# Kernel optimization log

Measured on AMD Instinct MI355X. Metric: run time of the kernel, lower is better.

## Reference

```python
import jax, jax.numpy as jnp
import numpy as np
from functools import partial

N_NODES = 100000
N_REL = 3
N_EDGES = 200000
IN_F = 128
HID_F = 128
OUT_F = 128
N_QUERY = 4096


def _graph_conv(x, es, ed, W, b, n_nodes):
    """DGL GraphConv with norm='both': D_dst^{-1/2} A D_src^{-1/2} X W + b.
    es/ed: [E] int edge endpoints, x: [N, d_in], W: [d_in, d_out], b: [d_out]."""
    ones = jnp.ones(es.shape[0], dtype=x.dtype)
    out_deg = jnp.clip(jax.ops.segment_sum(ones, es, num_segments=n_nodes), 1.0)
    in_deg = jnp.clip(jax.ops.segment_sum(ones, ed, num_segments=n_nodes), 1.0)
    # transform first (dense GEMM), then gather -> scatter-add over dst
    y = (x * jax.lax.rsqrt(out_deg)[:, None]) @ W          # [N, d_out]
    msg = y[es]                                            # [E, d_out] gather
    agg = jax.ops.segment_sum(msg, ed, num_segments=n_nodes)  # [N, d_out]
    return agg * jax.lax.rsqrt(in_deg)[:, None] + b


def _hetero_layer(x, e_src, e_dst, W, b, n_nodes):
    # HeteroGraphConv(aggregate='sum'): sum per-relation GraphConv outputs.
    out = _graph_conv(x, e_src[0], e_dst[0], W[0], b[0], n_nodes)
    for r in range(1, e_src.shape[0]):
        out = out + _graph_conv(x, e_src[r], e_dst[r], W[r], b[r], n_nodes)
    return out


def setup_inputs() -> dict:
    key = jax.random.key(0)
    ks = jax.random.split(key, 9)
    s = 1.0 / np.sqrt(IN_F)
    return {
        "emb": jax.random.normal(ks[0], (N_NODES, IN_F), jnp.float32),
        "W1": jax.random.normal(ks[1], (N_REL, IN_F, HID_F), jnp.float32) * s,
        "b1": jnp.zeros((N_REL, HID_F), jnp.float32),
        "W2": jax.random.normal(ks[2], (N_REL, HID_F, OUT_F), jnp.float32) * s,
        "b2": jnp.zeros((N_REL, OUT_F), jnp.float32),
        "e_src": jax.random.randint(ks[3], (N_REL, N_EDGES), 0, N_NODES, jnp.int32),
        "e_dst": jax.random.randint(ks[4], (N_REL, N_EDGES), 0, N_NODES, jnp.int32),
        "src": jax.random.randint(ks[5], (N_QUERY,), 0, N_NODES, jnp.int32),
        "dst": jax.random.randint(ks[6], (N_QUERY,), 0, N_NODES, jnp.int32),
    }


def reference(emb, W1, b1, W2, b2, e_src, e_dst, src, dst):
    n = emb.shape[0]
    h = jnp.tanh(_hetero_layer(emb, e_src, e_dst, W1, b1, n))
    h = jnp.tanh(_hetero_layer(h, e_src, e_dst, W2, b2, n))
    return (h[src], h[dst])
```

## Files before the change

### kernel.cpp

```cpp
#include <hip/hip_runtime.h>
#include <stdint.h>

#define NN 100000
#define NREL 3
#define NE 200000
#define F 128
#define NQ 4096

#define NBUCK (NREL * NN)
#define NCB ((NBUCK + 255) / 256)
#define CH_BLOCKS 512
#define CH_CHUNK ((NREL * NE + CH_BLOCKS - 1) / CH_BLOCKS)

#define WCVT_N (2 * NREL * F * F)
#define A1 (WCVT_N + 256)
#define A2 (A1 + NN * F / 8)
#define A3 (A2 + 2 * NQ)
#define A4 (A3 + NN)
#define A5 (A4 + NN)
#define PREP_N (A5 + 1)
#define PREP_BLKS ((PREP_N + 255) / 256)

typedef float fx4 __attribute__((ext_vector_type(4)));
typedef unsigned short u16x8 __attribute__((ext_vector_type(8)));
typedef __bf16 bf16x8 __attribute__((ext_vector_type(8)));

__device__ __forceinline__ unsigned short f2bf(float f) {
  uint32_t u = __builtin_bit_cast(uint32_t, f);
  uint32_t r = u + 0x7FFFu + ((u >> 16) & 1u);
  return (unsigned short)(r >> 16);
}
__device__ __forceinline__ float bf2f(unsigned short u) {
  return __builtin_bit_cast(float, (uint32_t)u << 16);
}
__device__ __forceinline__ int rel_of(int i) {
  return (i >= 2 * NE) ? 2 : (i >= NE ? 1 : 0);
}

__global__ __launch_bounds__(256) void prepch_kernel(
    const float* __restrict__ W1, const float* __restrict__ W2,
    const float* __restrict__ b1, const float* __restrict__ b2,
    const float* __restrict__ emb,
    const int* __restrict__ qsrc, const int* __restrict__ qdst,
    const int* __restrict__ es, const int* __restrict__ ed,
    unsigned short* __restrict__ Wtb, float* __restrict__ bsum,
    unsigned short* __restrict__ xb,
    int* __restrict__ qnode, int* __restrict__ mark, int* __restrict__ qflag,
    int* __restrict__ cursor,
    int* __restrict__ Hd, int* __restrict__ Hs) {
  __shared__ int hd[NCB], hs[NCB];
  int t = threadIdx.x;
  if (blockIdx.x >= PREP_BLKS) {
    int blk = blockIdx.x - PREP_BLKS;
    for (int j = t; j < NCB; j += 256) { hd[j] = 0; hs[j] = 0; }
    __syncthreads();
    int lo = blk * CH_CHUNK;
    int hi = min(lo + CH_CHUNK, NREL * NE);
    for (int i = lo + t; i < hi; i += 256) {
      int r = rel_of(i);
      atomicAdd(&hd[(r * NN + ed[i]) >> 8], 1);
      atomicAdd(&hs[(r * NN + es[i]) >> 8], 1);
    }
    __syncthreads();
    for (int j = t; j < NCB; j += 256) {
      Hd[blk * NCB + j] = hd[j];
      Hs[blk * NCB + j] = hs[j];
    }
    return;
  }
  int i = blockIdx.x * blockDim.x + t;
  if (i < WCVT_N) {
    int l = i / (NREL * F * F);
    int rem = i % (NREL * F * F);
    int r = rem / (F * F);
    int nk = rem % (F * F);
    int n = nk >> 7, k = nk & 127;
    const float* W = l ? W2 : W1;
    Wtb[i] = f2bf(W[r * F * F + k * F + n]);
  } else if (i < A1) {
    int tt = i - WCVT_N;
    int l = tt >> 7, f = tt & 127;
    const float* b = l ? b2 : b1;
    bsum[l * F + f] = b[f] + b[F + f] + b[2 * F + f];
  } else if (i < A2) {
    int j = i - A1;
    const float* p = emb + (size_t)j * 8;
    unsigned short tmp[8];
#pragma unroll
    for (int e = 0; e < 8; ++e) tmp[e] = f2bf(p[e]);
    *reinterpret_cast<u16x8*>(xb + (size_t)j * 8) = *reinterpret_cast<u16x8*>(tmp);
  } else if (i < A3) {
    int m = i - A2;
    qnode[m] = (m < NQ) ? qsrc[m] : qdst[m - NQ];
  } else if (i < A4) {
    mark[i - A3] = 0;
  } else if (i < A5) {
    qflag[i - A4] = 0;
  } else if (i < PREP_N) {
    *cursor = 0;
  }
}

__global__ __launch_bounds__(256) void hsum_kernel(const int* __restrict__ Hd,
                                                   const int* __restrict__ Hs,
                                                   const int* __restrict__ qnode,
                                                   int* __restrict__ chist_d,
                                                   int* __restrict__ chist_s,
                                                   int* __restrict__ qflag) {
  int t = threadIdx.x, lane = t & 63;
  int q = blockIdx.x * 256 + t;
  if (q < 2 * NQ) qflag[qnode[q]] = 1;
  int ws = blockIdx.x * 4 + (t >> 6);
  if (ws >= 2 * NCB) return;
  const int* H = (ws < NCB) ? Hd : Hs;
  int bin = (ws < NCB) ? ws : ws - NCB;
  int s = 0;
#pragma unroll
  for (int k = 0; k < 8; ++k) s += H[(size_t)(lane * 8 + k) * NCB + bin];
#pragma unroll
  for (int d = 1; d < 64; d <<= 1) s += __shfl_xor(s, d);
  if (lane == 0) {
    if (ws < NCB) chist_d[bin] = s; else chist_s[bin] = s;
  }
}

__global__ __launch_bounds__(256) void cscan_kernel(const int* __restrict__ chist_d,
                                                    const int* __restrict__ chist_s,
                                                    int* __restrict__ cstart_d,
                                                    int* __restrict__ cstart_s) {
  const int* chist = blockIdx.x ? chist_s : chist_d;
  int* cstart = blockIdx.x ? cstart_s : cstart_d;
  int t = threadIdx.x, lane = t & 63, w = t >> 6;
  int v[5];
  int s = 0;
#pragma unroll
  for (int k = 0; k < 5; ++k) {
    int i = t * 5 + k;
    v[k] = (i < NCB) ? chist[i] : 0;
    s += v[k];
  }
  int sc = s;
#pragma unroll
  for (int d = 1; d < 64; d <<= 1) {
    int o = __shfl_up(sc, d);
    if (lane >= d) sc += o;
  }
  __shared__ int wt[4];
  if (lane == 63) wt[w] = sc;
  __syncthreads();
  int woff = 0;
#pragma unroll
  for (int ww = 0; ww < 3; ++ww) woff += (ww < w) ? wt[ww] : 0;
  int excl = woff + sc - s;
#pragma unroll
  for (int k = 0; k < 5; ++k) {
    int i = t * 5 + k;
    if (i < NCB) { cstart[i] = excl; excl += v[k]; }
  }
}

__global__ __launch_bounds__(256) void hbase_kernel(const int* __restrict__ Hd,
                                                    const int* __restrict__ Hs,
                                                    const int* __restrict__ cstart_d,
                                                    const int* __restrict__ cstart_s,
                                                    int* __restrict__ Hbase_d,
                                                    int* __restrict__ Hbase_s) {
  const int* H = blockIdx.y ? Hs : Hd;
  const int* cstart = blockIdx.y ? cstart_s : cstart_d;
  int* Hbase = blockIdx.y ? Hbase_s : Hbase_d;
  int t = threadIdx.x, lane = t & 63;
  int bin = blockIdx.x * 4 + (t >> 6);
  int v[8];
  int s = 0;
#pragma unroll
  for (int k = 0; k < 8; ++k) {
    v[k] = H[(size_t)(lane * 8 + k) * NCB + bin];
    s += v[k];
  }
  int sc = s;
#pragma unroll
  for (int d = 1; d < 64; d <<= 1) {
    int o = __shfl_up(sc, d);
    if (lane >= d) sc += o;
  }
  int run = cstart[bin] + sc - s;
#pragma unroll
  for (int k = 0; k < 8; ++k) {
    Hbase[bin * CH_BLOCKS + lane * 8 + k] = run;
    run += v[k];
  }
}

__global__ __launch_bounds__(256) void cscatter_kernel(const int* __restrict__ es,
                                                       const int* __restrict__ ed,
                                                       const int* __restrict__ Hbase_d,
                                                       const int* __restrict__ Hbase_s,
                                                       int* __restrict__ etmp_d,
                                                       int* __restrict__ etmp_s) {
  __shared__ int cur_d[NCB], cur_s[NCB];
  int t = threadIdx.x, blk = blockIdx.x;
  for (int j = t; j < NCB; j += 256) {
    cur_d[j] = Hbase_d[j * CH_BLOCKS + blk];
    cur_s[j] = Hbase_s[j * CH_BLOCKS + blk];
  }
  __syncthreads();
  int lo = blk * CH_CHUNK;
  int hi = min(lo + CH_CHUNK, NREL * NE);
  for (int i = lo + t; i < hi; i += 256) {
    int r = rel_of(i);
    int s = es[i], d = ed[i];
    int bd = r * NN + d;
    int pos = atomicAdd(&cur_d[bd >> 8], 1);
    etmp_d[pos] = (s << 8) | (bd & 255);
    int bs = r * NN + s;
    int pos_s = atomicAdd(&cur_s[bs >> 8], 1);
    etmp_s[pos_s] = bs & 255;
  }
}

__global__ __launch_bounds__(256) void srccount_kernel(const int* __restrict__ etmp_s,
                                                       const int* __restrict__ cstart_s,
                                                       const int* __restrict__ chist_s,
                                                       int* __restrict__ cnt_src) {
  const int cb = blockIdx.x;
  const int t = threadIdx.x;
  const int cs = cstart_s[cb], cc = chist_s[cb];
  __shared__ int fcnt[256];
  fcnt[t] = 0;
  __syncthreads();
  for (int i = t; i < cc; i += 256) atomicAdd(&fcnt[etmp_s[cs + i]], 1);
  __syncthreads();
  int b = cb * 256 + t;
  if (b < NBUCK) cnt_src[b] = fcnt[t];
}

__global__ __launch_bounds__(256) void fine_kernel(const int* __restrict__ etmp,
                                                   const int* __restrict__ cstart,
                                                   const int* __restrict__ chist,
                                                   const int* __restrict__ cnt_src,
                                                   const int* __restrict__ qflag,
                                                   int2* __restrict__ scb,
                                                   int2* __restrict__ epay,
                                                   int* __restrict__ mark) {
  const int cb = blockIdx.x;
  const int t = threadIdx.x, lane = t & 63, w = t >> 6;
  const int cs = cstart[cb], cc = chist[cb];
  __shared__ int fcnt[256], fexcl[256], fcur[256];
  fcnt[t] = 0;
  fcur[t] = 0;
  __syncthreads();
  for (int i = t; i < cc; i += 256) atomicAdd(&fcnt[etmp[cs + i] & 255], 1);
  __syncthreads();
  int val = fcnt[t];
  int sc = val;
#pragma unroll
  for (int d = 1; d < 64; d <<= 1) {
    int o = __shfl_up(sc, d);
    if (lane >= d) sc += o;
  }
  __shared__ int wt[4];
  if (lane == 63) wt[w] = sc;
  __syncthreads();
  int woff = 0;
#pragma unroll
  for (int ww = 0; ww < 3; ++ww) woff += (ww < w) ? wt[ww] : 0;
  fexcl[t] = woff + sc - val;
  int b = cb * 256 + t;
  if (b < NBUCK) scb[b] = make_int2(cs + fexcl[t], val);
  __syncthreads();
  for (int i = t; i < cc; i += 256) {
    int e = etmp[cs + i];
    int f = e & 255;
    int src = ((unsigned)e) >> 8;
    int fine = cb * 256 + f;
    int r = fine / NN;
    int dst = fine - r * NN;
    float wgt = rsqrtf((float)cnt_src[r * NN + src]) * rsqrtf((float)fcnt[f]);
    int pos = cs + fexcl[f] + atomicAdd(&fcur[f], 1);
    epay[pos] = make_int2(src, __builtin_bit_cast(int, wgt));
    if (qflag[dst]) mark[src] = 1;
  }
}

__global__ __launch_bounds__(256) void compact_kernel(const int* __restrict__ mark,
                                                      int* __restrict__ list,
                                                      int* __restrict__ cursor) {
  int t = threadIdx.x, lane = t & 63, w = t >> 6;
  int base = blockIdx.x * 1024 + t * 4;
  int loc[4];
  int cnt = 0;
#pragma unroll
  for (int k = 0; k < 4; ++k) {
    int i = base + k;
    if (i < NN && mark[i]) { loc[cnt] = i; ++cnt; }
  }
  int sc = cnt;
#pragma unroll
  for (int d = 1; d < 64; d <<= 1) {
    int o = __shfl_up(sc, d);
    if (lane >= d) sc += o;
  }
  int texcl = sc - cnt;
  __shared__ int wt[4];
  __shared__ int bb;
  if (lane == 63) wt[w] = sc;
  __syncthreads();
  if (t == 0) {
    int tot = wt[0] + wt[1] + wt[2] + wt[3];
    bb = atomicAdd(cursor, tot);
    int a = 0;
#pragma unroll
    for (int ww = 0; ww < 4; ++ww) { int c = wt[ww]; wt[ww] = a; a += c; }
  }
  __syncthreads();
  int p = bb + wt[w] + texcl;
  for (int k = 0; k < cnt; ++k) list[p + k] = loc[k];
}

__global__ __launch_bounds__(256) void aggz_kernel(const unsigned short* __restrict__ X,
                                                   const int2* __restrict__ scb,
                                                   const int2* __restrict__ epay,
                                                   const int* __restrict__ nmap,
                                                   const int* __restrict__ cntp,
                                                   unsigned short* __restrict__ Z,
                                                   int Mcap, int Ms) {
  const int count = cntp ? *cntp : Mcap;
  const int r = blockIdx.y;
  const int t = threadIdx.x;
  const int lane = t & 63;
  const int m = blockIdx.x * 16 + (t >> 6) * 4 + (lane >> 4);
  const int j = lane & 15;
  if (m >= count) return;
  int n = nmap ? nmap[m] : m;
  int2 meta = scb[r * NN + n];
  const int2* ep = epay + meta.x;
  const int c = meta.y;

  float ps[8];
#pragma unroll
  for (int k = 0; k < 8; ++k) ps[k] = 0.f;

  int i = 0;
  for (; i + 2 <= c; i += 2) {
    int2 p0 = ep[i], p1 = ep[i + 1];
    float w0 = __builtin_bit_cast(float, p0.y);
    float w1 = __builtin_bit_cast(float, p1.y);
    u16x8 v0 = *reinterpret_cast<const u16x8*>(X + ((size_t)p0.x << 7) + j * 8);
    u16x8 v1 = *reinterpret_cast<const u16x8*>(X + ((size_t)p1.x << 7) + j * 8);
#pragma unroll
    for (int k = 0; k < 8; ++k)
      ps[k] = fmaf(bf2f(v1[k]), w1, fmaf(bf2f(v0[k]), w0, ps[k]));
  }
  if (i < c) {
    int2 p0 = ep[i];
    float w0 = __builtin_bit_cast(float, p0.y);
    u16x8 v0 = *reinterpret_cast<const u16x8*>(X + ((size_t)p0.x << 7) + j * 8);
#pragma unroll
    for (int k = 0; k < 8; ++k) ps[k] = fmaf(bf2f(v0[k]), w0, ps[k]);
  }

  unsigned short tmp[8];
#pragma unroll
  for (int k = 0; k < 8; ++k) tmp[k] = f2bf(ps[k]);
  *reinterpret_cast<u16x8*>(Z + (((size_t)r * Ms + m) << 7) + j * 8) =
      *reinterpret_cast<u16x8*>(tmp);
}

#define GBM 128
__global__ __launch_bounds__(512) void gemmp_kernel(const unsigned short* __restrict__ Z,
                                                    const unsigned short* __restrict__ Wt3,
                                                    const float* __restrict__ bsum,
                                                    const int* __restrict__ omap,
                                                    const int* __restrict__ cntp,
                                                    void* __restrict__ outp,
                                                    int M, int Ms, int out_f32) {
  const int count = cntp ? *cntp : M;
  const int m0 = blockIdx.x * GBM;
  if (m0 >= count) return;
  __shared__ unsigned short Abuf[2][GBM * F];
  const int t = threadIdx.x;
  const int lane = t & 63, w = t >> 6;
  const int wm = w >> 2, wn = w & 3;
  const int r0 = lane & 15, kq = lane >> 4;

  fx4 acc[4][2];
#pragma unroll
  for (int mt = 0; mt < 4; ++mt)
#pragma unroll
    for (int nt = 0; nt < 2; ++nt) acc[mt][nt] = (fx4){0.f, 0.f, 0.f, 0.f};

  {
    const unsigned short* Zr = Z + (size_t)m0 * F;
#pragma unroll
    for (int i = 0; i < 4; ++i) {
      int slot = i * 512 + t;
      int row = slot >> 4, s = slot & 15;
      __builtin_amdgcn_global_load_lds(
          (const __attribute__((address_space(1))) uint32_t*)(
              Zr + ((size_t)row << 7) + ((s ^ (row & 7)) << 3)),
          (__attribute__((address_space(3))) uint32_t*)&Abuf[0][slot * 8], 16, 0, 0);
    }
  }
  __syncthreads();

  int cur = 0;
  for (int r = 0; r < NREL; ++r) {
    bf16x8 bfrag[2][4];
    const unsigned short* Wt = Wt3 + (size_t)r * F * F;
#pragma unroll
    for (int nt = 0; nt < 2; ++nt)
#pragma unroll
      for (int kb = 0; kb < 4; ++kb)
        bfrag[nt][kb] = __builtin_bit_cast(bf16x8,
            *reinterpret_cast<const u16x8*>(
                Wt + (wn * 32 + nt * 16 + r0) * F + (4 * kb + kq) * 8));

    if (r + 1 < NREL) {
      const unsigned short* Zr = Z + ((size_t)(r + 1) * Ms + m0) * F;
#pragma unroll
      for (int i = 0; i < 4; ++i) {
        int slot = i * 512 + t;
        int row = slot >> 4, s = slot & 15;
        __builtin_amdgcn_global_load_lds(
            (const __attribute__((address_space(1))) uint32_t*)(
                Zr + ((size_t)row << 7) + ((s ^ (row & 7)) << 3)),
            (__attribute__((address_space(3))) uint32_t*)&Abuf[cur ^ 1][slot * 8],
            16, 0, 0);
      }
    }

#pragma unroll
    for (int kb = 0; kb < 4; ++kb) {
      const int cs = ((kb * 4 + kq) ^ (r0 & 7)) * 8;
      bf16x8 a[4];
#pragma unroll
      for (int mt = 0; mt < 4; ++mt)
        a[mt] = __builtin_bit_cast(bf16x8,
            *reinterpret_cast<const u16x8*>(&Abuf[cur][(wm * 64 + mt * 16 + r0) * F + cs]));
#pragma unroll
      for (int mt = 0; mt < 4; ++mt)
#pragma unroll
        for (int nt = 0; nt < 2; ++nt)
          acc[mt][nt] = __builtin_amdgcn_mfma_f32_16x16x32_bf16(a[mt], bfrag[nt][kb],
                                                                acc[mt][nt], 0, 0, 0);
    }

    __syncthreads();
    cur ^= 1;
  }

#pragma unroll
  for (int mt = 0; mt < 4; ++mt) {
    const int rbase = m0 + wm * 64 + mt * 16 + kq * 4;
#pragma unroll
    for (int nt = 0; nt < 2; ++nt) {
      int col = wn * 32 + nt * 16 + r0;
      float bb = bsum[col];
#pragma unroll
      for (int reg = 0; reg < 4; ++reg) {
        int gm = rbase + reg;
        if (gm < count) {
          float v = tanhf(acc[mt][nt][reg] + bb);
          if (omap) {
            ((unsigned short*)outp)[(size_t)omap[gm] * F + col] = f2bf(v);
          } else if (out_f32) {
            ((float*)outp)[(size_t)gm * F + col] = v;
          } else {
            ((unsigned short*)outp)[(size_t)gm * F + col] = f2bf(v);
          }
        }
      }
    }
  }
}

extern "C" void kernel_launch(void* const* d_in, const int* in_sizes, int n_in,
                              void* d_out, int out_size, void* d_ws, size_t ws_size,
                              hipStream_t stream) {
  const float* emb = (const float*)d_in[0];
  const float* W1  = (const float*)d_in[1];
  const float* b1  = (const float*)d_in[2];
  const float* W2  = (const float*)d_in[3];
  const float* b2  = (const float*)d_in[4];
  const int* e_src = (const int*)d_in[5];
  const int* e_dst = (const int*)d_in[6];
  const int* qsrc  = (const int*)d_in[7];
  const int* qdst  = (const int*)d_in[8];
  float* out = (float*)d_out;

  const int MS1 = ((NN + GBM - 1) / GBM) * GBM;
  const int MQ  = 2 * NQ;

  char* p = (char*)d_ws;
  size_t off = 0;
  auto take = [&](size_t n) { void* q = p + off; off = (off + n + 255) & ~(size_t)255; return q; };
  int* cnt_src  = (int*)take((size_t)NREL * NN * 4);
  int* chist_d  = (int*)take((size_t)NCB * 4);
  int* chist_s  = (int*)take((size_t)NCB * 4);
  int* cstart_d = (int*)take((size_t)NCB * 4);
  int* cstart_s = (int*)take((size_t)NCB * 4);
  int* Hd       = (int*)take((size_t)NCB * CH_BLOCKS * 4);
  int* Hs       = (int*)take((size_t)NCB * CH_BLOCKS * 4);
  int* Hbase_d  = (int*)take((size_t)NCB * CH_BLOCKS * 4);
  int* Hbase_s  = (int*)take((size_t)NCB * CH_BLOCKS * 4);
  int* etmp_d   = (int*)take((size_t)NREL * NE * 4);
  int* etmp_s   = (int*)take((size_t)NREL * NE * 4);
  int2* scb     = (int2*)take((size_t)NBUCK * 8);
  int2* epay    = (int2*)take((size_t)NREL * NE * 8);
  unsigned short* Wtb = (unsigned short*)take(2ull * NREL * F * F * 2);
  float* bsum   = (float*)take(2ull * F * 4);
  int* qnode    = (int*)take((size_t)MQ * 4);
  int* mark     = (int*)take((size_t)NN * 4);
  int* qflag    = (int*)take((size_t)NN * 4);
  int* list     = (int*)take((size_t)NN * 4 + 4);
  int* cursor   = (int*)take(4);
  unsigned short* Xb  = (unsigned short*)take((size_t)NN * F * 2);
  unsigned short* Xb2 = (unsigned short*)take((size_t)NN * F * 2);
  unsigned short* Z   = (unsigned short*)take((size_t)NREL * MS1 * F * 2);

  prepch_kernel<<<PREP_BLKS + CH_BLOCKS, 256, 0, stream>>>(
      W1, W2, b1, b2, emb, qsrc, qdst, e_src, e_dst,
      Wtb, bsum, Xb, qnode, mark, qflag, cursor, Hd, Hs);
  hsum_kernel<<<(2 * NCB + 3) / 4, 256, 0, stream>>>(Hd, Hs, qnode,
                                                     chist_d, chist_s, qflag);
  cscan_kernel<<<2, 256, 0, stream>>>(chist_d, chist_s, cstart_d, cstart_s);
  {
    dim3 hb(NCB / 4, 2);
    hbase_kernel<<<hb, 256, 0, stream>>>(Hd, Hs, cstart_d, cstart_s, Hbase_d, Hbase_s);
  }
  cscatter_kernel<<<CH_BLOCKS, 256, 0, stream>>>(e_src, e_dst, Hbase_d, Hbase_s,
                                                 etmp_d, etmp_s);
  srccount_kernel<<<NCB, 256, 0, stream>>>(etmp_s, cstart_s, chist_s, cnt_src);
  fine_kernel<<<NCB, 256, 0, stream>>>(etmp_d, cstart_d, chist_d, cnt_src, qflag,
                                       scb, epay, mark);
  compact_kernel<<<(NN + 1023) / 1024, 256, 0, stream>>>(mark, list, cursor);

  dim3 ag1((NN + 15) / 16, NREL);
  aggz_kernel<<<ag1, 256, 0, stream>>>(Xb, scb, epay, list, cursor, Z, NN, MS1);
  gemmp_kernel<<<MS1 / GBM, 512, 0, stream>>>(Z, Wtb, bsum, list, cursor, Xb2, MS1, MS1, 0);

  dim3 ag2((MQ + 15) / 16, NREL);
  aggz_kernel<<<ag2, 256, 0, stream>>>(Xb2, scb, epay, qnode, nullptr, Z, MQ, MQ);
  gemmp_kernel<<<MQ / GBM, 512, 0, stream>>>(
      Z, Wtb + (size_t)NREL * F * F, bsum + F, nullptr, nullptr, out, MQ, MQ, 1);
}
```

Baseline: 148.6 us.

## Fold histogram column sums into scan kernel and shrink counting-sort block count

Cuts the counting-sort chunk blocks from 512 to 128, shrinking the per-block histogram matrix by a factor of four. That makes it small enough to drop the separate hsum kernel. The scan kernel now sums each bin's column across all chunk blocks itself, and a third block sets the query flags. This saves a launch and traffic on the histogram, but the column sums now run in only two blocks with long serial loops. The scatter pass also loses parallelism, since each of its 128 blocks handles a much larger edge chunk.

```diff
diff --git a/kernel.cpp b/kernel.cpp
--- a/kernel.cpp
+++ b/kernel.cpp
@@ -9,7 +9,7 @@
 
 #define NBUCK (NREL * NN)
 #define NCB ((NBUCK + 255) / 256)
-#define CH_BLOCKS 512
+#define CH_BLOCKS 128
 #define CH_CHUNK ((NREL * NE + CH_BLOCKS - 1) / CH_BLOCKS)
 
 #define WCVT_N (2 * NREL * F * F)
@@ -101,43 +101,34 @@
   }
 }
 
-__global__ __launch_bounds__(256) void hsum_kernel(const int* __restrict__ Hd,
-                                                   const int* __restrict__ Hs,
-                                                   const int* __restrict__ qnode,
-                                                   int* __restrict__ chist_d,
-                                                   int* __restrict__ chist_s,
-                                                   int* __restrict__ qflag) {
-  int t = threadIdx.x, lane = t & 63;
-  int q = blockIdx.x * 256 + t;
-  if (q < 2 * NQ) qflag[qnode[q]] = 1;
-  int ws = blockIdx.x * 4 + (t >> 6);
-  if (ws >= 2 * NCB) return;
-  const int* H = (ws < NCB) ? Hd : Hs;
-  int bin = (ws < NCB) ? ws : ws - NCB;
-  int s = 0;
-#pragma unroll
-  for (int k = 0; k < 8; ++k) s += H[(size_t)(lane * 8 + k) * NCB + bin];
-#pragma unroll
-  for (int d = 1; d < 64; d <<= 1) s += __shfl_xor(s, d);
-  if (lane == 0) {
-    if (ws < NCB) chist_d[bin] = s; else chist_s[bin] = s;
-  }
-}
-
-__global__ __launch_bounds__(256) void cscan_kernel(const int* __restrict__ chist_d,
-                                                    const int* __restrict__ chist_s,
+__global__ __launch_bounds__(256) void cscan_kernel(const int* __restrict__ Hd,
+                                                    const int* __restrict__ Hs,
+                                                    const int* __restrict__ qnode,
+                                                    int* __restrict__ chist_d,
+                                                    int* __restrict__ chist_s,
                                                     int* __restrict__ cstart_d,
-                                                    int* __restrict__ cstart_s) {
-  const int* chist = blockIdx.x ? chist_s : chist_d;
+                                                    int* __restrict__ cstart_s,
+                                                    int* __restrict__ qflag) {
+  int t = threadIdx.x, lane = t & 63, w = t >> 6;
+  if (blockIdx.x == 2) {
+    for (int q = t; q < 2 * NQ; q += 256) qflag[qnode[q]] = 1;
+    return;
+  }
+  const int* H = blockIdx.x ? Hs : Hd;
+  int* chist = blockIdx.x ? chist_s : chist_d;
   int* cstart = blockIdx.x ? cstart_s : cstart_d;
-  int t = threadIdx.x, lane = t & 63, w = t >> 6;
   int v[5];
   int s = 0;
 #pragma unroll
   for (int k = 0; k < 5; ++k) {
     int i = t * 5 + k;
-    v[k] = (i < NCB) ? chist[i] : 0;
-    s += v[k];
+    int sum = 0;
+    if (i < NCB) {
+      for (int b = 0; b < CH_BLOCKS; ++b) sum += H[(size_t)b * NCB + i];
+      chist[i] = sum;
+    }
+    v[k] = sum;
+    s += sum;
   }
   int sc = s;
 #pragma unroll
@@ -170,11 +161,11 @@
   int* Hbase = blockIdx.y ? Hbase_s : Hbase_d;
   int t = threadIdx.x, lane = t & 63;
   int bin = blockIdx.x * 4 + (t >> 6);
-  int v[8];
+  int v[2];
   int s = 0;
 #pragma unroll
-  for (int k = 0; k < 8; ++k) {
-    v[k] = H[(size_t)(lane * 8 + k) * NCB + bin];
+  for (int k = 0; k < 2; ++k) {
+    v[k] = H[(size_t)(lane * 2 + k) * NCB + bin];
     s += v[k];
   }
   int sc = s;
@@ -185,8 +176,8 @@
   }
   int run = cstart[bin] + sc - s;
 #pragma unroll
-  for (int k = 0; k < 8; ++k) {
-    Hbase[bin * CH_BLOCKS + lane * 8 + k] = run;
+  for (int k = 0; k < 2; ++k) {
+    Hbase[bin * CH_BLOCKS + lane * 2 + k] = run;
     run += v[k];
   }
 }
@@ -521,9 +512,8 @@
   prepch_kernel<<<PREP_BLKS + CH_BLOCKS, 256, 0, stream>>>(
       W1, W2, b1, b2, emb, qsrc, qdst, e_src, e_dst,
       Wtb, bsum, Xb, qnode, mark, qflag, cursor, Hd, Hs);
-  hsum_kernel<<<(2 * NCB + 3) / 4, 256, 0, stream>>>(Hd, Hs, qnode,
-                                                     chist_d, chist_s, qflag);
-  cscan_kernel<<<2, 256, 0, stream>>>(chist_d, chist_s, cstart_d, cstart_s);
+  cscan_kernel<<<3, 256, 0, stream>>>(Hd, Hs, qnode, chist_d, chist_s,
+                                      cstart_d, cstart_s, qflag);
   {
     dim3 hb(NCB / 4, 2);
     hbase_kernel<<<hb, 256, 0, stream>>>(Hd, Hs, cstart_d, cstart_s, Hbase_d, Hbase_s);
```

Measured after the change: 157.8 us. 6.3% more time.
